# Kernel optimization log

Hardware: AMD Instinct MI355X
Metric: run time of the kernel (lower is better)

The kernel has to match this reference:

```python
import jax, jax.numpy as jnp
import numpy as np

D = 128
N = 262144

def setup_inputs() -> dict:
    key = jax.random.key(0)
    ks = jax.random.split(key, 10)
    inp = {
        'member_embeddings': 0.1 * jax.random.normal(ks[0], (N, D), dtype=jnp.float32),
        'item_embedding': 0.1 * jax.random.normal(ks[1], (D,), dtype=jnp.float32),
        # nn.Linear params (torch convention: y = x @ W.T + b)
        'W_c1': jax.random.normal(ks[2], (D, D), dtype=jnp.float32) / np.sqrt(D),
        'b_c1': jnp.zeros((D,), dtype=jnp.float32),
        'W_c2': jax.random.normal(ks[3], (D, D), dtype=jnp.float32) / np.sqrt(D),
        'b_c2': jnp.zeros((D,), dtype=jnp.float32),
        'w_pa': jax.random.normal(ks[4], (D,), dtype=jnp.float32) / np.sqrt(D),  # peer_attention weight (1,D) squeezed
        'b_pa': jnp.zeros((), dtype=jnp.float32),
        'w_vc': jax.random.normal(ks[5], (D,), dtype=jnp.float32) / np.sqrt(D),  # v_c weight (1,D) squeezed
        'b_vc': jnp.zeros((), dtype=jnp.float32),
    }
    return inp

def reference(member_embeddings, item_embedding, W_c1, b_c1, W_c2, b_c2, w_pa, b_pa, w_vc, b_vc):
    E = member_embeddings  # [N, D]
    # SP: self persistence scores  alpha_SP_i = u_i^T v
    sp = E @ item_embedding  # [N]
    # Peer scores are per-member scalars shared across all exclusion sets.
    s = E @ w_pa + b_pa                       # [N]
    m = jnp.max(s)
    e = jnp.exp(s - m)                        # [N]
    S = jnp.sum(e)                            # scalar
    eE = e[:, None] * E                       # [N, D]
    sum_eE = jnp.sum(eE, axis=0)              # [D]
    # softmax over peers excluding i (exact: softmax is shift-invariant)
    denom = S - e                             # [N]
    peer_agg = (sum_eE[None, :] - eE) / denom[:, None]  # [N, D]
    # PI: v_c^T ReLU(W_c1 u_i + W_c2 peer_agg_i + b)
    h = E @ W_c1.T + b_c1 + peer_agg @ W_c2.T + b_c2     # [N, D]
    pi = jax.nn.relu(h) @ w_vc + b_vc                    # [N]  (dropout = identity in eval)
    alpha = jnp.float32(1.0)
    beta = jnp.float32(1.0)
    attention_weights = jax.nn.softmax(alpha * sp + beta * pi, axis=0)  # [N]
    group_embedding = attention_weights @ E               # [D]
    return (group_embedding, attention_weights)
```

## Files before the change

kernel.cpp:

```cpp
#include <hip/hip_runtime.h>

#define DIM 128

typedef __attribute__((ext_vector_type(8))) short bf16x8;
typedef __attribute__((ext_vector_type(4))) float f32x4;

#define WS_B12    0
#define WS_C      128
#define WS_SUMEE  256
#define WS_S      384
#define WS_ZB     416
#define WS_GEB    512
#define WS_WBF    4608
#define WS_EEP    20992
#define WS_SEP    152064
#define WS_SP     153088
#define WS_E      415232
#define WS_WEXP   677376

__device__ __forceinline__ unsigned short f2bf(float f) {
    union { float f; unsigned u; } v; v.f = f;
    unsigned r = v.u + 0x7fffu + ((v.u >> 16) & 1u);
    return (unsigned short)(r >> 16);
}

__device__ __forceinline__ float bfbits(unsigned u) {
    union { unsigned u; float f; } v; v.u = u;
    return v.f;
}

__global__ __launch_bounds__(256) void k1_init(const float* __restrict__ Wc1,
                                               const float* __restrict__ Wc2,
                                               const float* __restrict__ bc1,
                                               const float* __restrict__ bc2,
                                               float* __restrict__ ws) {
    int gid = blockIdx.x * 256 + threadIdx.x;
    unsigned short* wbf = (unsigned short*)(ws + WS_WBF);
    if (gid < 32768) {
        int n = gid >> 7, k = gid & 127;
        float v = (n < 128) ? Wc1[n * 128 + k] : Wc2[(n - 128) * 128 + k];
        wbf[gid] = f2bf(v);
    }
    if (gid < 4096) ws[WS_GEB + gid] = 0.f;
    if (gid < 128) ws[WS_B12 + gid] = bc1[gid] + bc2[gid];
    if (gid < 64) ws[WS_ZB + gid] = 0.f;
}

__global__ __launch_bounds__(256) void k2_stats(const float* __restrict__ E,
                                                const float* __restrict__ v,
                                                const float* __restrict__ wpa,
                                                const float* __restrict__ bpa,
                                                float* __restrict__ ws) {
    __shared__ float red[16][128];
    __shared__ float redS[16];
    int t = threadIdx.x;
    int wave = t >> 6, lane = t & 63;
    int cl = lane & 15, rs = lane >> 4;
    int row0 = blockIdx.x * 256;
    const float4* E4 = (const float4*)E;

    float4 va = ((const float4*)v)[cl];
    float4 vb = ((const float4*)v)[16 + cl];
    float4 pa = ((const float4*)wpa)[cl];
    float4 pb = ((const float4*)wpa)[16 + cl];
    float bias = bpa[0];

    float4 acc0 = {0.f, 0.f, 0.f, 0.f}, acc1 = {0.f, 0.f, 0.f, 0.f};
    float se = 0.f;
    float* sp_ws = ws + WS_SP;
    float* e_ws = ws + WS_E;

#pragma unroll 4
    for (int it = 0; it < 16; ++it) {
        int row = row0 + it * 16 + wave * 4 + rs;
        float4 x0 = E4[row * 32 + cl];
        float4 x1 = E4[row * 32 + 16 + cl];
        float dv = x0.x * va.x + x0.y * va.y + x0.z * va.z + x0.w * va.w
                 + x1.x * vb.x + x1.y * vb.y + x1.z * vb.z + x1.w * vb.w;
        float dp = x0.x * pa.x + x0.y * pa.y + x0.z * pa.z + x0.w * pa.w
                 + x1.x * pb.x + x1.y * pb.y + x1.z * pb.z + x1.w * pb.w;
        for (int off = 1; off < 16; off <<= 1) {
            dv += __shfl_xor(dv, off);
            dp += __shfl_xor(dp, off);
        }
        float e = __expf(dp + bias);
        if (cl == 0) {
            sp_ws[row] = dv;
            e_ws[row] = e;
            se += e;
        }
        acc0.x += e * x0.x; acc0.y += e * x0.y; acc0.z += e * x0.z; acc0.w += e * x0.w;
        acc1.x += e * x1.x; acc1.y += e * x1.y; acc1.z += e * x1.z; acc1.w += e * x1.w;
    }
    int rr = wave * 4 + rs;
    float* dst = red[rr];
    dst[cl * 4 + 0] = acc0.x; dst[cl * 4 + 1] = acc0.y;
    dst[cl * 4 + 2] = acc0.z; dst[cl * 4 + 3] = acc0.w;
    dst[64 + cl * 4 + 0] = acc1.x; dst[64 + cl * 4 + 1] = acc1.y;
    dst[64 + cl * 4 + 2] = acc1.z; dst[64 + cl * 4 + 3] = acc1.w;
    if (cl == 0) redS[rr] = se;
    __syncthreads();
    if (t < 128) {
        float s = 0.f;
#pragma unroll
        for (int r = 0; r < 16; ++r) s += red[r][t];
        ws[WS_EEP + t * 1024 + blockIdx.x] = s;
    }
    if (t == 0) {
        float s = 0.f;
#pragma unroll
        for (int r = 0; r < 16; ++r) s += redS[r];
        ws[WS_SEP + blockIdx.x] = s;
    }
}

__global__ __launch_bounds__(256) void k2b_reduce(float* __restrict__ ws) {
    __shared__ float r4[4];
    int t = threadIdx.x, blk = blockIdx.x;
    const float* src = (blk < 128) ? (ws + WS_EEP + blk * 1024) : (ws + WS_SEP);
    float s = src[t] + src[t + 256] + src[t + 512] + src[t + 768];
    for (int off = 1; off < 64; off <<= 1) s += __shfl_xor(s, off);
    if ((t & 63) == 0) r4[t >> 6] = s;
    __syncthreads();
    if (t == 0) {
        float tot = r4[0] + r4[1] + r4[2] + r4[3];
        if (blk < 128) ws[WS_SUMEE + blk] = tot;
        else ws[WS_S] = tot;
    }
}

__global__ __launch_bounds__(128) void k3_c(const float* __restrict__ Wc2,
                                            float* __restrict__ ws) {
    int j = threadIdx.x;
    const float4* row = (const float4*)(Wc2 + j * 128);
    const float4* se = (const float4*)(ws + WS_SUMEE);
    float4 s4 = {0.f, 0.f, 0.f, 0.f};
#pragma unroll
    for (int k = 0; k < 32; ++k) {
        float4 a = row[k], b = se[k];
        s4.x += a.x * b.x; s4.y += a.y * b.y; s4.z += a.z * b.z; s4.w += a.w * b.w;
    }
    ws[WS_C + j] = s4.x + s4.y + s4.z + s4.w;
}

__global__ __launch_bounds__(512, 6) void k4_main(const float* __restrict__ E,
                                                  const float* __restrict__ wvc,
                                                  const float* __restrict__ bvc_p,
                                                  float* __restrict__ ws) {
    __shared__ unsigned short Elds[64 * 136];
    __shared__ float pim[8][64];
    __shared__ float gep[8][128];
    __shared__ float e_lds[64], dinv_lds[64];
    __shared__ float zw[8];

    int t = threadIdx.x;
    int w = t >> 6, lane = t & 63, cl = lane & 15, q = lane >> 4;
    int row0 = blockIdx.x * 64;
    const unsigned short* wbf = (const unsigned short*)(ws + WS_WBF);

    int j = w * 16 + cl;
    float cj = ws[WS_C + j];
    float b12j = ws[WS_B12 + j];
    float wvcj = wvc[j];
    float bvc = bvc_p[0];
    int r0 = w * 8 + q * 2;
    float sp0 = ws[WS_SP + row0 + r0];
    float sp1 = ws[WS_SP + row0 + r0 + 1];

    bf16x8 bfr[2][4];
#pragma unroll
    for (int c2 = 0; c2 < 2; ++c2) {
        int ct = w + c2 * 8;
#pragma unroll
        for (int kt = 0; kt < 4; ++kt)
            bfr[c2][kt] = *(const bf16x8*)(wbf + (ct * 16 + cl) * 128 + kt * 32 + q * 8);
    }

    const float4* E4 = (const float4*)E + (size_t)row0 * 32;
#pragma unroll
    for (int i = 0; i < 4; ++i) {
        int idx = t + 512 * i;
        int row = idx >> 5, kq = idx & 31;
        float4 x = E4[idx];
        unsigned p0 = (unsigned)f2bf(x.x) | ((unsigned)f2bf(x.y) << 16);
        unsigned p1 = (unsigned)f2bf(x.z) | ((unsigned)f2bf(x.w) << 16);
        *(uint2*)&Elds[row * 136 + kq * 4] = make_uint2(p0, p1);
    }
    if (t < 64) {
        float Sv = ws[WS_S];
        float ev = ws[WS_E + row0 + t];
        e_lds[t] = ev;
        dinv_lds[t] = 1.0f / (Sv - ev);
    }
    __syncthreads();

    f32x4 acc[4][2];
#pragma unroll
    for (int rt = 0; rt < 4; ++rt) {
        acc[rt][0] = (f32x4){0.f, 0.f, 0.f, 0.f};
        acc[rt][1] = (f32x4){0.f, 0.f, 0.f, 0.f};
    }
#pragma unroll
    for (int rt = 0; rt < 4; ++rt) {
        bf16x8 a[4];
#pragma unroll
        for (int kt = 0; kt < 4; ++kt)
            a[kt] = *(const bf16x8*)&Elds[(rt * 16 + cl) * 136 + kt * 32 + q * 8];
#pragma unroll
        for (int kt = 0; kt < 4; ++kt) {
            acc[rt][0] = __builtin_amdgcn_mfma_f32_16x16x32_bf16(a[kt], bfr[0][kt], acc[rt][0], 0, 0, 0);
            acc[rt][1] = __builtin_amdgcn_mfma_f32_16x16x32_bf16(a[kt], bfr[1][kt], acc[rt][1], 0, 0, 0);
        }
    }

#pragma unroll
    for (int rt = 0; rt < 4; ++rt) {
#pragma unroll
        for (int reg = 0; reg < 4; ++reg) {
            int row_it = rt * 16 + q * 4 + reg;
            float er = e_lds[row_it];
            float dinv = dinv_lds[row_it];
            float h = acc[rt][0][reg] + b12j + (cj - er * acc[rt][1][reg]) * dinv;
            float p = wvcj * fmaxf(h, 0.f);
            p += __shfl_xor(p, 1);
            p += __shfl_xor(p, 2);
            p += __shfl_xor(p, 4);
            p += __shfl_xor(p, 8);
            if (cl == 0) pim[w][row_it] = p;
        }
    }
    __syncthreads();

    float pi0 = 0.f, pi1 = 0.f;
#pragma unroll
    for (int wv = 0; wv < 8; ++wv) {
        pi0 += pim[wv][r0];
        pi1 += pim[wv][r0 + 1];
    }
    float we0 = __expf(sp0 + bvc + pi0);
    float we1 = __expf(sp1 + bvc + pi1);
    if (cl == 0) {
        ws[WS_WEXP + row0 + r0] = we0;
        ws[WS_WEXP + row0 + r0 + 1] = we1;
    }
    float z = we0 + we1;
    z += __shfl_xor(z, 16);
    z += __shfl_xor(z, 32);
    if (lane == 0) zw[w] = z;

    float acc8[8] = {0.f, 0.f, 0.f, 0.f, 0.f, 0.f, 0.f, 0.f};
#pragma unroll
    for (int rr = 0; rr < 2; ++rr) {
        int r = r0 + rr;
        float wer = rr ? we1 : we0;
        uint4 u = *(const uint4*)&Elds[r * 136 + cl * 8];
        acc8[0] += wer * bfbits(u.x << 16);
        acc8[1] += wer * bfbits(u.x & 0xffff0000u);
        acc8[2] += wer * bfbits(u.y << 16);
        acc8[3] += wer * bfbits(u.y & 0xffff0000u);
        acc8[4] += wer * bfbits(u.z << 16);
        acc8[5] += wer * bfbits(u.z & 0xffff0000u);
        acc8[6] += wer * bfbits(u.w << 16);
        acc8[7] += wer * bfbits(u.w & 0xffff0000u);
    }
#pragma unroll
    for (int jj = 0; jj < 8; ++jj) {
        acc8[jj] += __shfl_xor(acc8[jj], 16);
        acc8[jj] += __shfl_xor(acc8[jj], 32);
    }
    if (lane < 16) {
        *(float4*)&gep[w][cl * 8] = (float4){acc8[0], acc8[1], acc8[2], acc8[3]};
        *(float4*)&gep[w][cl * 8 + 4] = (float4){acc8[4], acc8[5], acc8[6], acc8[7]};
    }
    __syncthreads();

    if (t < 128) {
        float tot = 0.f;
#pragma unroll
        for (int wv = 0; wv < 8; ++wv) tot += gep[wv][t];
        atomicAdd(&ws[WS_GEB + (blockIdx.x & 31) * 128 + t], tot);
    }
    if (t == 128) {
        float zs = zw[0] + zw[1] + zw[2] + zw[3] + zw[4] + zw[5] + zw[6] + zw[7];
        atomicAdd(&ws[WS_ZB + (blockIdx.x & 63)], zs);
    }
}

__global__ __launch_bounds__(256) void k5_final(const float* __restrict__ ws,
                                                float* __restrict__ out) {
    int t = threadIdx.x, blk = blockIdx.x;
    float z = ws[WS_ZB + (t & 63)];
    for (int off = 1; off < 64; off <<= 1) z += __shfl_xor(z, off);
    float invZ = 1.0f / z;
    if (blk < 1024) {
        int i = blk * 256 + t;
        out[128 + i] = ws[WS_WEXP + i] * invZ;
    } else if (t < 128) {
        float s = 0.f;
#pragma unroll
        for (int b = 0; b < 32; ++b) s += ws[WS_GEB + b * 128 + t];
        out[t] = s * invZ;
    }
}

extern "C" void kernel_launch(void* const* d_in, const int* in_sizes, int n_in,
                              void* d_out, int out_size, void* d_ws, size_t ws_size,
                              hipStream_t stream) {
    const float* E   = (const float*)d_in[0];
    const float* v   = (const float*)d_in[1];
    const float* Wc1 = (const float*)d_in[2];
    const float* bc1 = (const float*)d_in[3];
    const float* Wc2 = (const float*)d_in[4];
    const float* bc2 = (const float*)d_in[5];
    const float* wpa = (const float*)d_in[6];
    const float* bpa = (const float*)d_in[7];
    const float* wvc = (const float*)d_in[8];
    const float* bvc = (const float*)d_in[9];
    float* ws  = (float*)d_ws;
    float* out = (float*)d_out;

    k1_init<<<128, 256, 0, stream>>>(Wc1, Wc2, bc1, bc2, ws);
    k2_stats<<<1024, 256, 0, stream>>>(E, v, wpa, bpa, ws);
    k2b_reduce<<<129, 256, 0, stream>>>(ws);
    k3_c<<<1, 128, 0, stream>>>(Wc2, ws);
    k4_main<<<4096, 512, 0, stream>>>(E, wvc, bvc, ws);
    k5_final<<<1025, 256, 0, stream>>>(ws, out);
}
```

Measured before the change: 274.6 us.

## Precompute bf16 copy of E in stats pass and drop LDS staging in main

After: 344.7 us. +25.5%, slower.

```diff
diff --git a/kernel.cpp b/kernel.cpp
--- a/kernel.cpp
+++ b/kernel.cpp
@@ -17,6 +17,7 @@
 #define WS_SP     153088
 #define WS_E      415232
 #define WS_WEXP   677376
+#define WS_EBF    939520
 
 __device__ __forceinline__ unsigned short f2bf(float f) {
     union { float f; unsigned u; } v; v.f = f;
@@ -29,35 +30,35 @@
     return v.f;
 }
 
-__global__ __launch_bounds__(256) void k1_init(const float* __restrict__ Wc1,
-                                               const float* __restrict__ Wc2,
-                                               const float* __restrict__ bc1,
-                                               const float* __restrict__ bc2,
-                                               float* __restrict__ ws) {
-    int gid = blockIdx.x * 256 + threadIdx.x;
-    unsigned short* wbf = (unsigned short*)(ws + WS_WBF);
-    if (gid < 32768) {
-        int n = gid >> 7, k = gid & 127;
-        float v = (n < 128) ? Wc1[n * 128 + k] : Wc2[(n - 128) * 128 + k];
-        wbf[gid] = f2bf(v);
-    }
-    if (gid < 4096) ws[WS_GEB + gid] = 0.f;
-    if (gid < 128) ws[WS_B12 + gid] = bc1[gid] + bc2[gid];
-    if (gid < 64) ws[WS_ZB + gid] = 0.f;
-}
-
 __global__ __launch_bounds__(256) void k2_stats(const float* __restrict__ E,
                                                 const float* __restrict__ v,
                                                 const float* __restrict__ wpa,
                                                 const float* __restrict__ bpa,
+                                                const float* __restrict__ Wc1,
+                                                const float* __restrict__ Wc2,
+                                                const float* __restrict__ bc1,
+                                                const float* __restrict__ bc2,
                                                 float* __restrict__ ws) {
     __shared__ float red[16][128];
     __shared__ float redS[16];
     int t = threadIdx.x;
+
+    int gid = blockIdx.x * 256 + t;
+    unsigned short* wbf_w = (unsigned short*)(ws + WS_WBF);
+    if (gid < 32768) {
+        int n = gid >> 7, k = gid & 127;
+        float val = (n < 128) ? Wc1[n * 128 + k] : Wc2[(n - 128) * 128 + k];
+        wbf_w[gid] = f2bf(val);
+    }
+    if (gid < 4096) ws[WS_GEB + gid] = 0.f;
+    if (gid < 128) ws[WS_B12 + gid] = bc1[gid] + bc2[gid];
+    if (gid < 64) ws[WS_ZB + gid] = 0.f;
+
     int wave = t >> 6, lane = t & 63;
     int cl = lane & 15, rs = lane >> 4;
     int row0 = blockIdx.x * 256;
     const float4* E4 = (const float4*)E;
+    unsigned short* ebf = (unsigned short*)(ws + WS_EBF);
 
     float4 va = ((const float4*)v)[cl];
     float4 vb = ((const float4*)v)[16 + cl];
@@ -75,6 +76,13 @@
         int row = row0 + it * 16 + wave * 4 + rs;
         float4 x0 = E4[row * 32 + cl];
         float4 x1 = E4[row * 32 + 16 + cl];
+        unsigned p0 = (unsigned)f2bf(x0.x) | ((unsigned)f2bf(x0.y) << 16);
+        unsigned p1 = (unsigned)f2bf(x0.z) | ((unsigned)f2bf(x0.w) << 16);
+        unsigned p2 = (unsigned)f2bf(x1.x) | ((unsigned)f2bf(x1.y) << 16);
+        unsigned p3 = (unsigned)f2bf(x1.z) | ((unsigned)f2bf(x1.w) << 16);
+        *(uint2*)(ebf + (size_t)row * 128 + cl * 4) = make_uint2(p0, p1);
+        *(uint2*)(ebf + (size_t)row * 128 + 64 + cl * 4) = make_uint2(p2, p3);
+
         float dv = x0.x * va.x + x0.y * va.y + x0.z * va.z + x0.w * va.w
                  + x1.x * vb.x + x1.y * vb.y + x1.z * vb.z + x1.w * vb.w;
         float dp = x0.x * pa.x + x0.y * pa.y + x0.z * pa.z + x0.w * pa.w
@@ -143,11 +151,9 @@
     ws[WS_C + j] = s4.x + s4.y + s4.z + s4.w;
 }
 
-__global__ __launch_bounds__(512, 6) void k4_main(const float* __restrict__ E,
-                                                  const float* __restrict__ wvc,
+__global__ __launch_bounds__(512, 4) void k4_main(const float* __restrict__ wvc,
                                                   const float* __restrict__ bvc_p,
                                                   float* __restrict__ ws) {
-    __shared__ unsigned short Elds[64 * 136];
     __shared__ float pim[8][64];
     __shared__ float gep[8][128];
     __shared__ float e_lds[64], dinv_lds[64];
@@ -157,6 +163,7 @@
     int w = t >> 6, lane = t & 63, cl = lane & 15, q = lane >> 4;
     int row0 = blockIdx.x * 64;
     const unsigned short* wbf = (const unsigned short*)(ws + WS_WBF);
+    const unsigned short* Eb = (const unsigned short*)(ws + WS_EBF) + (size_t)row0 * 128;
 
     int j = w * 16 + cl;
     float cj = ws[WS_C + j];
@@ -176,23 +183,12 @@
             bfr[c2][kt] = *(const bf16x8*)(wbf + (ct * 16 + cl) * 128 + kt * 32 + q * 8);
     }
 
-    const float4* E4 = (const float4*)E + (size_t)row0 * 32;
-#pragma unroll
-    for (int i = 0; i < 4; ++i) {
-        int idx = t + 512 * i;
-        int row = idx >> 5, kq = idx & 31;
-        float4 x = E4[idx];
-        unsigned p0 = (unsigned)f2bf(x.x) | ((unsigned)f2bf(x.y) << 16);
-        unsigned p1 = (unsigned)f2bf(x.z) | ((unsigned)f2bf(x.w) << 16);
-        *(uint2*)&Elds[row * 136 + kq * 4] = make_uint2(p0, p1);
-    }
     if (t < 64) {
         float Sv = ws[WS_S];
         float ev = ws[WS_E + row0 + t];
         e_lds[t] = ev;
         dinv_lds[t] = 1.0f / (Sv - ev);
     }
-    __syncthreads();
 
     f32x4 acc[4][2];
 #pragma unroll
@@ -205,13 +201,15 @@
         bf16x8 a[4];
 #pragma unroll
         for (int kt = 0; kt < 4; ++kt)
-            a[kt] = *(const bf16x8*)&Elds[(rt * 16 + cl) * 136 + kt * 32 + q * 8];
+            a[kt] = *(const bf16x8*)(Eb + (rt * 16 + cl) * 128 + kt * 32 + q * 8);
 #pragma unroll
         for (int kt = 0; kt < 4; ++kt) {
             acc[rt][0] = __builtin_amdgcn_mfma_f32_16x16x32_bf16(a[kt], bfr[0][kt], acc[rt][0], 0, 0, 0);
             acc[rt][1] = __builtin_amdgcn_mfma_f32_16x16x32_bf16(a[kt], bfr[1][kt], acc[rt][1], 0, 0, 0);
         }
     }
+
+    __syncthreads();
 
 #pragma unroll
     for (int rt = 0; rt < 4; ++rt) {
@@ -253,7 +251,7 @@
     for (int rr = 0; rr < 2; ++rr) {
         int r = r0 + rr;
         float wer = rr ? we1 : we0;
-        uint4 u = *(const uint4*)&Elds[r * 136 + cl * 8];
+        uint4 u = *(const uint4*)(Eb + r * 128 + cl * 8);
         acc8[0] += wer * bfbits(u.x << 16);
         acc8[1] += wer * bfbits(u.x & 0xffff0000u);
         acc8[2] += wer * bfbits(u.y << 16);
@@ -319,10 +317,9 @@
     float* ws  = (float*)d_ws;
     float* out = (float*)d_out;
 
-    k1_init<<<128, 256, 0, stream>>>(Wc1, Wc2, bc1, bc2, ws);
-    k2_stats<<<1024, 256, 0, stream>>>(E, v, wpa, bpa, ws);
+    k2_stats<<<1024, 256, 0, stream>>>(E, v, wpa, bpa, Wc1, Wc2, bc1, bc2, ws);
     k2b_reduce<<<129, 256, 0, stream>>>(ws);
     k3_c<<<1, 128, 0, stream>>>(Wc2, ws);
-    k4_main<<<4096, 512, 0, stream>>>(E, wvc, bvc, ws);
+    k4_main<<<4096, 512, 0, stream>>>(wvc, bvc, ws);
     k5_final<<<1025, 256, 0, stream>>>(ws, out);
 }
```
